# Kernel tuning notes

Hardware: AMD Instinct MI355X
Metric: run time of the kernel (lower is better)

The kernel has to match this reference:

```python
import jax, jax.numpy as jnp
import numpy as np

EMBED = 1024
HEAD = 128

def setup_inputs() -> dict:
    key = jax.random.key(0)
    k1, k2, k3, k4 = jax.random.split(key, 4)
    x = jax.random.normal(k1, (4, 4096, EMBED), dtype=jnp.float32)
    # nn.Linear default init ~ U(-1/sqrt(fan_in), 1/sqrt(fan_in)); weights stored as [in, out] for x @ W
    s = 1.0 / np.sqrt(EMBED)
    Wq = jax.random.uniform(k2, (EMBED, HEAD), dtype=jnp.float32, minval=-s, maxval=s)
    Wk = jax.random.uniform(k3, (EMBED, HEAD), dtype=jnp.float32, minval=-s, maxval=s)
    Wv = jax.random.uniform(k4, (EMBED, HEAD), dtype=jnp.float32, minval=-s, maxval=s)
    return {"x": x, "Wq": Wq, "Wk": Wk, "Wv": Wv}

def reference(x, Wq, Wk, Wv):
    # x: [B, S, E]
    B, S, E = x.shape
    q = x @ Wq  # [B, S, H]
    k = x @ Wk
    v = x @ Wv
    scale = jnp.asarray(k.shape[-1], x.dtype) ** -0.5
    scores = jnp.einsum('bqh,bkh->bqk', q, k) * scale  # [B, S, S]
    causal = jnp.tril(jnp.ones((S, S), dtype=bool))
    scores = jnp.where(causal, scores, jnp.asarray(-jnp.inf, x.dtype))
    attn = jax.nn.softmax(scores, axis=-1)
    return jnp.einsum('bqk,bkh->bqh', attn, v)  # [B, S, H]
```

## Files before the change

kernel.cpp:

```cpp
#include <hip/hip_runtime.h>
#include <math.h>

#define BATCH 4
#define SEQ   4096
#define EMB   1024
#define HD    128
#define MROWS (BATCH*SEQ)
#define SCALE 0.08838834764831844f
#define NJOBS 204
#define MAXC  6

typedef __attribute__((ext_vector_type(8))) short bf16x8;
typedef __attribute__((ext_vector_type(4))) short short4v;
typedef __attribute__((ext_vector_type(4))) float f32x4;
typedef __attribute__((ext_vector_type(4))) int   i32x4;

static __device__ __forceinline__ unsigned short f2bf(float f) {
    unsigned int u = __float_as_uint(f);
    u += 0x7fff + ((u >> 16) & 1);
    return (unsigned short)(u >> 16);
}
static __device__ __forceinline__ float bf2f(unsigned short s) {
    return __uint_as_float((unsigned int)s << 16);
}

__global__ __launch_bounds__(128) void wtrans_kernel(
    const float* __restrict__ Wq, const float* __restrict__ Wk,
    const float* __restrict__ Wv, unsigned short* __restrict__ Wt)
{
    const int w  = blockIdx.y;
    const float* W = (w == 0) ? Wq : (w == 1) ? Wk : Wv;
    const float sc = (w == 0) ? SCALE : 1.0f;
    unsigned short* dst = Wt + (size_t)w * 131072;
    const int n  = threadIdx.x;
    const int k0 = blockIdx.x * 64;
    for (int jc = 0; jc < 8; ++jc) {
        i32x4 p;
#pragma unroll
        for (int e = 0; e < 4; ++e) {
            float lo = W[(size_t)(k0 + jc * 8 + e * 2)     * HD + n] * sc;
            float hi = W[(size_t)(k0 + jc * 8 + e * 2 + 1) * HD + n] * sc;
            p[e] = (unsigned int)f2bf(lo) | ((unsigned int)f2bf(hi) << 16);
        }
        *(i32x4*)&dst[(size_t)n * 1024 + k0 + jc * 8] = p;
    }
}

__global__ __launch_bounds__(512, 4) void qkv_kernel(
    const float* __restrict__ x, const unsigned short* __restrict__ Wt,
    unsigned short* __restrict__ qb, unsigned short* __restrict__ kb,
    unsigned short* __restrict__ vtb)
{
    __shared__ __align__(16) unsigned short lds[32 * 72 + 384 * 72];
    unsigned short* xs = lds;
    unsigned short* Ws = lds + 32 * 72;

    const int t    = threadIdx.x;
    const int lane = t & 63, ng = t >> 6;
    const int quad = lane >> 4, l16 = lane & 15;
    const int m0   = blockIdx.x * 32;

    f32x4 acc[2][3];
#pragma unroll
    for (int i = 0; i < 2; ++i)
#pragma unroll
        for (int j = 0; j < 3; ++j) acc[i][j] = (f32x4){0.f, 0.f, 0.f, 0.f};

    const int xrow = t >> 4, xc4 = t & 15;
    const int wrow = t >> 3, wseg = t & 7;

    for (int kt = 0; kt < EMB; kt += 64) {
        __syncthreads();
        {
            float4 xa = *(const float4*)&x[(size_t)(m0 + xrow) * EMB + kt + xc4 * 4];
            short4v xcv;
            xcv[0] = (short)f2bf(xa.x); xcv[1] = (short)f2bf(xa.y);
            xcv[2] = (short)f2bf(xa.z); xcv[3] = (short)f2bf(xa.w);
            *(short4v*)&xs[xrow * 72 + xc4 * 4] = xcv;
        }
#pragma unroll
        for (int i = 0; i < 6; ++i) {
            int row = i * 64 + wrow;
            *(i32x4*)&Ws[row * 72 + wseg * 8] =
                *(const i32x4*)&Wt[(size_t)row * 1024 + kt + wseg * 8];
        }
        __syncthreads();
#pragma unroll
        for (int ks = 0; ks < 2; ++ks) {
            bf16x8 aA[2], aB[3];
#pragma unroll
            for (int mt = 0; mt < 2; ++mt)
                aA[mt] = *(const bf16x8*)&xs[(mt * 16 + l16) * 72 + ks * 32 + quad * 8];
#pragma unroll
            for (int jt = 0; jt < 3; ++jt)
                aB[jt] = *(const bf16x8*)&Ws[((ng * 3 + jt) * 16 + l16) * 72 + ks * 32 + quad * 8];
#pragma unroll
            for (int mt = 0; mt < 2; ++mt)
#pragma unroll
                for (int jt = 0; jt < 3; ++jt)
                    acc[mt][jt] = __builtin_amdgcn_mfma_f32_16x16x32_bf16(
                        aA[mt], aB[jt], acc[mt][jt], 0, 0, 0);
        }
    }

    __syncthreads();
    unsigned short* Cq = lds;
    unsigned short* Ck = lds + 32 * 136;
    unsigned short* Cv = lds + 2 * 32 * 136;
#pragma unroll
    for (int mt = 0; mt < 2; ++mt)
#pragma unroll
        for (int jt = 0; jt < 3; ++jt) {
            int nt = ng * 3 + jt;
            int wm = nt >> 3, nl = nt & 7;
            if (wm < 2) {
                unsigned short* C = (wm == 0) ? Cq : Ck;
#pragma unroll
                for (int rr = 0; rr < 4; ++rr)
                    C[(mt * 16 + quad * 4 + rr) * 136 + nl * 16 + l16] =
                        f2bf(acc[mt][jt][rr]);
            } else {
                short4v p;
                p[0] = (short)f2bf(acc[mt][jt][0]); p[1] = (short)f2bf(acc[mt][jt][1]);
                p[2] = (short)f2bf(acc[mt][jt][2]); p[3] = (short)f2bf(acc[mt][jt][3]);
                *(short4v*)&Cv[(nl * 16 + l16) * 40 + mt * 16 + quad * 4] = p;
            }
        }
    __syncthreads();
    {
        int row = t >> 4, seg = t & 15;
        *(i32x4*)&qb[((size_t)(m0 + row)) * HD + seg * 8] = *(const i32x4*)&Cq[row * 136 + seg * 8];
        *(i32x4*)&kb[((size_t)(m0 + row)) * HD + seg * 8] = *(const i32x4*)&Ck[row * 136 + seg * 8];
    }
    {
        const int b = m0 >> 12, s0 = m0 & 4095;
        int h = t >> 2, seg = t & 3;
        *(i32x4*)&vtb[(size_t)b * (HD * SEQ) + (size_t)h * SEQ + s0 + seg * 8] =
            *(const i32x4*)&Cv[h * 40 + seg * 8];
    }
}

#define PADK 136
#define PADV 72
#define PADP 72

__global__ __launch_bounds__(256, 3) void flash_kernel(
    const unsigned short* __restrict__ qb, const unsigned short* __restrict__ kb,
    const unsigned short* __restrict__ vtb, unsigned short* __restrict__ Opart,
    float* __restrict__ mbuf, float* __restrict__ lbuf)
{
    __shared__ __align__(16) unsigned short Ks[64 * PADK];
    __shared__ __align__(16) unsigned short Vt[128 * PADV];
    __shared__ __align__(16) unsigned short Pt[64 * PADP];

    const int t    = threadIdx.x;
    const int lane = t & 63, w = t >> 6;
    const int quad = lane >> 4, l16 = lane & 15;
    const int b    = blockIdx.y;

    const int j = blockIdx.x;
    int g = 0, s = 0;
#pragma unroll
    for (int gg = 0; gg < 5; ++gg)
        if (j >= s + 12 * (g + 1)) { s += 12 * (g + 1); ++g; }
    const int idx = j - s;
    const int qi  = 12 * g + idx / (g + 1);
    const int c   = idx % (g + 1);

    const int qrow = qi * 64 + w * 16 + l16;
    const int jbeg = c * 12;
    const int jend = min(jbeg + 12, qi + 1);

    bf16x8 qf[4];
    {
        const unsigned short* qp = qb + ((size_t)b * SEQ + qrow) * HD;
#pragma unroll
        for (int ks = 0; ks < 4; ++ks)
            qf[ks] = *(const bf16x8*)&qp[ks * 32 + quad * 8];
    }

    f32x4 O[8];
#pragma unroll
    for (int i = 0; i < 8; ++i) O[i] = (f32x4){0.f, 0.f, 0.f, 0.f};
    float m_run = -1e30f, l_run = 0.f;

    const unsigned short* kbb  = kb  + (size_t)b * SEQ * HD;
    const unsigned short* vtbb = vtb + (size_t)b * HD * SEQ;

    for (int j0 = jbeg; j0 < jend; ++j0) {
        __syncthreads();
#pragma unroll
        for (int i = 0; i < 4; ++i) {
            int gg = i * 256 + t;
            i32x4 kd = *(const i32x4*)&kbb[(size_t)j0 * 64 * HD + (size_t)gg * 8];
            *(i32x4*)&Ks[(gg >> 4) * PADK + (gg & 15) * 8] = kd;
        }
#pragma unroll
        for (int i = 0; i < 4; ++i) {
            int gg = i * 256 + t;
            i32x4 vd = *(const i32x4*)&vtbb[(size_t)(gg >> 3) * SEQ + j0 * 64 + (gg & 7) * 8];
            *(i32x4*)&Vt[(gg >> 3) * PADV + (gg & 7) * 8] = vd;
        }
        __syncthreads();

        f32x4 st[4];
#pragma unroll
        for (int mt = 0; mt < 4; ++mt) {
            f32x4 a = (f32x4){0.f, 0.f, 0.f, 0.f};
#pragma unroll
            for (int ks = 0; ks < 4; ++ks) {
                bf16x8 kf = *(const bf16x8*)&Ks[(mt * 16 + l16) * PADK + ks * 32 + quad * 8];
                a = __builtin_amdgcn_mfma_f32_16x16x32_bf16(kf, qf[ks], a, 0, 0, 0);
            }
            st[mt] = a;
        }

        if (j0 * 64 + 63 > qi * 64 + w * 16) {
#pragma unroll
            for (int mt = 0; mt < 4; ++mt)
#pragma unroll
                for (int rr = 0; rr < 4; ++rr) {
                    int kv = j0 * 64 + mt * 16 + quad * 4 + rr;
                    if (kv > qrow) st[mt][rr] = -1e30f;
                }
        }

        float mx = -1e30f;
#pragma unroll
        for (int mt = 0; mt < 4; ++mt)
#pragma unroll
            for (int rr = 0; rr < 4; ++rr) mx = fmaxf(mx, st[mt][rr]);
        mx = fmaxf(mx, __shfl_xor(mx, 16));
        mx = fmaxf(mx, __shfl_xor(mx, 32));
        const float m_new = fmaxf(m_run, mx);
        const float alpha = __expf(m_run - m_new);
        float psum = 0.f;
#pragma unroll
        for (int mt = 0; mt < 4; ++mt)
#pragma unroll
            for (int rr = 0; rr < 4; ++rr) {
                float p = __expf(st[mt][rr] - m_new);
                st[mt][rr] = p;
                psum += p;
            }
        psum += __shfl_xor(psum, 16);
        psum += __shfl_xor(psum, 32);
        m_run = m_new;
        l_run = l_run * alpha + psum;

#pragma unroll
        for (int mt = 0; mt < 4; ++mt) {
            short4v p;
            p[0] = (short)f2bf(st[mt][0]); p[1] = (short)f2bf(st[mt][1]);
            p[2] = (short)f2bf(st[mt][2]); p[3] = (short)f2bf(st[mt][3]);
            *(short4v*)&Pt[(w * 16 + l16) * PADP + mt * 16 + quad * 4] = p;
        }

#pragma unroll
        for (int i = 0; i < 8; ++i) {
            O[i][0] *= alpha; O[i][1] *= alpha; O[i][2] *= alpha; O[i][3] *= alpha;
        }

        bf16x8 pf0 = *(const bf16x8*)&Pt[(w * 16 + l16) * PADP + quad * 8];
        bf16x8 pf1 = *(const bf16x8*)&Pt[(w * 16 + l16) * PADP + 32 + quad * 8];
#pragma unroll
        for (int mt = 0; mt < 8; ++mt) {
            bf16x8 vf0 = *(const bf16x8*)&Vt[(mt * 16 + l16) * PADV + quad * 8];
            bf16x8 vf1 = *(const bf16x8*)&Vt[(mt * 16 + l16) * PADV + 32 + quad * 8];
            O[mt] = __builtin_amdgcn_mfma_f32_16x16x32_bf16(vf0, pf0, O[mt], 0, 0, 0);
            O[mt] = __builtin_amdgcn_mfma_f32_16x16x32_bf16(vf1, pf1, O[mt], 0, 0, 0);
        }
    }

    const int r = w * 16 + l16;
    const size_t jobbase = (size_t)b * NJOBS + j;
    unsigned short* po = Opart + jobbase * (64 * 128) + (size_t)r * 128;
#pragma unroll
    for (int mt = 0; mt < 8; ++mt) {
        short4v p;
        p[0] = (short)f2bf(O[mt][0]); p[1] = (short)f2bf(O[mt][1]);
        p[2] = (short)f2bf(O[mt][2]); p[3] = (short)f2bf(O[mt][3]);
        *(short4v*)&po[mt * 16 + quad * 4] = p;
    }
    if (quad == 0) {
        mbuf[jobbase * 64 + r] = m_run;
        lbuf[jobbase * 64 + r] = l_run;
    }
}

__global__ __launch_bounds__(256) void combine_kernel(
    const unsigned short* __restrict__ Opart, const float* __restrict__ mbuf,
    const float* __restrict__ lbuf, float* __restrict__ out)
{
    const int qi = blockIdx.x, b = blockIdx.y;
    const int g  = qi / 12;
    const int nc = g + 1;
    const int j0 = 6 * g * (g + 1) + (qi - 12 * g) * (g + 1);
    const int t = threadIdx.x;
    const int row = t >> 2, cg = (t & 3) * 32;

    float mv[MAXC], lv[MAXC];
    float M = -1e30f;
    for (int c2 = 0; c2 < nc; ++c2) {
        const size_t jb = (size_t)b * NJOBS + j0 + c2;
        mv[c2] = mbuf[jb * 64 + row];
        lv[c2] = lbuf[jb * 64 + row];
        M = fmaxf(M, mv[c2]);
    }
    float L = 0.f;
    for (int c2 = 0; c2 < nc; ++c2) L += __expf(mv[c2] - M) * lv[c2];
    const float Linv = 1.0f / L;

    float acc[32];
#pragma unroll
    for (int i = 0; i < 32; ++i) acc[i] = 0.f;
    for (int c2 = 0; c2 < nc; ++c2) {
        const float wgt = __expf(mv[c2] - M) * Linv;
        const unsigned short* po = Opart + ((size_t)b * NJOBS + j0 + c2) * (64 * 128) +
                                   (size_t)row * 128 + cg;
#pragma unroll
        for (int i = 0; i < 4; ++i) {
            i32x4 d = *(const i32x4*)&po[i * 8];
#pragma unroll
            for (int e = 0; e < 4; ++e) {
                unsigned int u = (unsigned int)d[e];
                acc[i * 8 + e * 2]     = fmaf(wgt, bf2f((unsigned short)(u & 0xffff)), acc[i * 8 + e * 2]);
                acc[i * 8 + e * 2 + 1] = fmaf(wgt, bf2f((unsigned short)(u >> 16)),   acc[i * 8 + e * 2 + 1]);
            }
        }
    }
    float* op = out + ((size_t)b * SEQ + qi * 64 + row) * HD + cg;
#pragma unroll
    for (int i = 0; i < 8; ++i) {
        float4 res;
        res.x = acc[i * 4]; res.y = acc[i * 4 + 1];
        res.z = acc[i * 4 + 2]; res.w = acc[i * 4 + 3];
        *(float4*)&op[i * 4] = res;
    }
}

extern "C" void kernel_launch(void* const* d_in, const int* in_sizes, int n_in,
                              void* d_out, int out_size, void* d_ws, size_t ws_size,
                              hipStream_t stream) {
    const float* x  = (const float*)d_in[0];
    const float* Wq = (const float*)d_in[1];
    const float* Wk = (const float*)d_in[2];
    const float* Wv = (const float*)d_in[3];

    unsigned short* qb    = (unsigned short*)d_ws;
    unsigned short* kb    = qb  + (size_t)MROWS * HD;
    unsigned short* vtb   = kb  + (size_t)MROWS * HD;
    unsigned short* Wt    = vtb + (size_t)MROWS * HD;
    unsigned short* Opart = Wt  + (size_t)3 * HD * EMB;
    float* mbuf = (float*)(Opart + (size_t)BATCH * NJOBS * 64 * 128);
    float* lbuf = mbuf + (size_t)BATCH * NJOBS * 64;
    float* out = (float*)d_out;

    wtrans_kernel <<<dim3(16, 3),    dim3(128), 0, stream>>>(Wq, Wk, Wv, Wt);
    qkv_kernel    <<<dim3(512),      dim3(512), 0, stream>>>(x, Wt, qb, kb, vtb);
    flash_kernel  <<<dim3(NJOBS, 4), dim3(256), 0, stream>>>(qb, kb, vtb, Opart, mbuf, lbuf);
    combine_kernel<<<dim3(64, 4),    dim3(256), 0, stream>>>(Opart, mbuf, lbuf, out);
}
```

Measured before the change: 186.7 us.

## Use 128-row query tiles, double-buffer x in QKV, coalesce weight transpose

The flash kernel now processes 128 query rows per 512-thread block, so each loaded K/V tile is shared by twice as many queries. Work is split into 10-tile chunks with a new job mapping interleaved across batches, and warps skip tiles that lie entirely above the causal diagonal. The QKV projection double-buffers the x tile, prefetching the next slice during MFMA compute, and drops one barrier per iteration. The weight transpose goes through LDS for coalesced reads, and the combine kernel is adjusted to the new partition layout. Larger blocks may lower occupancy and leave the work per block less even.

```diff
diff --git a/kernel.cpp b/kernel.cpp
--- a/kernel.cpp
+++ b/kernel.cpp
@@ -7,8 +7,9 @@
 #define HD    128
 #define MROWS (BATCH*SEQ)
 #define SCALE 0.08838834764831844f
-#define NJOBS 204
-#define MAXC  6
+#define CHUNK 10
+#define NJOBS 119
+#define MAXC  7
 
 typedef __attribute__((ext_vector_type(8))) short bf16x8;
 typedef __attribute__((ext_vector_type(4))) short short4v;
@@ -24,26 +25,38 @@
     return __uint_as_float((unsigned int)s << 16);
 }
 
-__global__ __launch_bounds__(128) void wtrans_kernel(
+__global__ __launch_bounds__(256) void wtrans_kernel(
     const float* __restrict__ Wq, const float* __restrict__ Wk,
     const float* __restrict__ Wv, unsigned short* __restrict__ Wt)
 {
+    __shared__ __align__(16) unsigned short Xs[16 * 132];
     const int w  = blockIdx.y;
     const float* W = (w == 0) ? Wq : (w == 1) ? Wk : Wv;
     const float sc = (w == 0) ? SCALE : 1.0f;
     unsigned short* dst = Wt + (size_t)w * 131072;
-    const int n  = threadIdx.x;
-    const int k0 = blockIdx.x * 64;
-    for (int jc = 0; jc < 8; ++jc) {
-        i32x4 p;
-#pragma unroll
-        for (int e = 0; e < 4; ++e) {
-            float lo = W[(size_t)(k0 + jc * 8 + e * 2)     * HD + n] * sc;
-            float hi = W[(size_t)(k0 + jc * 8 + e * 2 + 1) * HD + n] * sc;
-            p[e] = (unsigned int)f2bf(lo) | ((unsigned int)f2bf(hi) << 16);
-        }
-        *(i32x4*)&dst[(size_t)n * 1024 + k0 + jc * 8] = p;
-    }
+    const int k0 = blockIdx.x * 16;
+    const int t  = threadIdx.x;
+
+#pragma unroll
+    for (int i = 0; i < 2; ++i) {
+        int gg = i * 256 + t;
+        int row = gg >> 5, c4 = gg & 31;
+        float4 a = *(const float4*)&W[(size_t)(k0 + row) * HD + c4 * 4];
+        short4v p;
+        p[0] = (short)f2bf(a.x * sc); p[1] = (short)f2bf(a.y * sc);
+        p[2] = (short)f2bf(a.z * sc); p[3] = (short)f2bf(a.w * sc);
+        *(short4v*)&Xs[row * 132 + c4 * 4] = p;
+    }
+    __syncthreads();
+    const int n = t >> 1, half = t & 1;
+    i32x4 o;
+#pragma unroll
+    for (int e = 0; e < 4; ++e) {
+        unsigned int lo = Xs[(half * 8 + e * 2    ) * 132 + n];
+        unsigned int hi = Xs[(half * 8 + e * 2 + 1) * 132 + n];
+        o[e] = (int)(lo | (hi << 16));
+    }
+    *(i32x4*)&dst[(size_t)n * 1024 + k0 + half * 8] = o;
 }
 
 __global__ __launch_bounds__(512, 4) void qkv_kernel(
@@ -51,9 +64,10 @@
     unsigned short* __restrict__ qb, unsigned short* __restrict__ kb,
     unsigned short* __restrict__ vtb)
 {
-    __shared__ __align__(16) unsigned short lds[32 * 72 + 384 * 72];
-    unsigned short* xs = lds;
-    unsigned short* Ws = lds + 32 * 72;
+    __shared__ __align__(16) unsigned short lds[2 * 2304 + 384 * 72];
+    unsigned short* xs0 = lds;
+    unsigned short* xs1 = lds + 2304;
+    unsigned short* Ws  = lds + 4608;
 
     const int t    = threadIdx.x;
     const int lane = t & 63, ng = t >> 6;
@@ -66,31 +80,45 @@
 #pragma unroll
         for (int j = 0; j < 3; ++j) acc[i][j] = (f32x4){0.f, 0.f, 0.f, 0.f};
 
-    const int xrow = t >> 4, xc4 = t & 15;
-    const int wrow = t >> 3, wseg = t & 7;
+    const int xrow = t >> 3, xseg = t & 7;
+    if (t < 256) {
+        float4 a = *(const float4*)&x[(size_t)(m0 + xrow) * EMB + xseg * 8];
+        float4 b2 = *(const float4*)&x[(size_t)(m0 + xrow) * EMB + xseg * 8 + 4];
+        i32x4 p;
+        p[0] = (int)((unsigned)f2bf(a.x) | ((unsigned)f2bf(a.y) << 16));
+        p[1] = (int)((unsigned)f2bf(a.z) | ((unsigned)f2bf(a.w) << 16));
+        p[2] = (int)((unsigned)f2bf(b2.x) | ((unsigned)f2bf(b2.y) << 16));
+        p[3] = (int)((unsigned)f2bf(b2.z) | ((unsigned)f2bf(b2.w) << 16));
+        *(i32x4*)&xs0[xrow * 72 + xseg * 8] = p;
+    }
+    __syncthreads();
 
     for (int kt = 0; kt < EMB; kt += 64) {
-        __syncthreads();
-        {
-            float4 xa = *(const float4*)&x[(size_t)(m0 + xrow) * EMB + kt + xc4 * 4];
-            short4v xcv;
-            xcv[0] = (short)f2bf(xa.x); xcv[1] = (short)f2bf(xa.y);
-            xcv[2] = (short)f2bf(xa.z); xcv[3] = (short)f2bf(xa.w);
-            *(short4v*)&xs[xrow * 72 + xc4 * 4] = xcv;
-        }
+        unsigned short* xb = (kt & 64) ? xs1 : xs0;
+        unsigned short* xn = (kt & 64) ? xs0 : xs1;
 #pragma unroll
         for (int i = 0; i < 6; ++i) {
-            int row = i * 64 + wrow;
-            *(i32x4*)&Ws[row * 72 + wseg * 8] =
-                *(const i32x4*)&Wt[(size_t)row * 1024 + kt + wseg * 8];
-        }
-        __syncthreads();
+            int rowl = ng * 48 + i * 8 + (lane >> 3);
+            int seg  = lane & 7;
+            *(i32x4*)&Ws[rowl * 72 + seg * 8] =
+                *(const i32x4*)&Wt[(size_t)rowl * 1024 + kt + seg * 8];
+        }
+        if (t < 256 && kt + 64 < EMB) {
+            float4 a = *(const float4*)&x[(size_t)(m0 + xrow) * EMB + kt + 64 + xseg * 8];
+            float4 b2 = *(const float4*)&x[(size_t)(m0 + xrow) * EMB + kt + 64 + xseg * 8 + 4];
+            i32x4 p;
+            p[0] = (int)((unsigned)f2bf(a.x) | ((unsigned)f2bf(a.y) << 16));
+            p[1] = (int)((unsigned)f2bf(a.z) | ((unsigned)f2bf(a.w) << 16));
+            p[2] = (int)((unsigned)f2bf(b2.x) | ((unsigned)f2bf(b2.y) << 16));
+            p[3] = (int)((unsigned)f2bf(b2.z) | ((unsigned)f2bf(b2.w) << 16));
+            *(i32x4*)&xn[xrow * 72 + xseg * 8] = p;
+        }
 #pragma unroll
         for (int ks = 0; ks < 2; ++ks) {
             bf16x8 aA[2], aB[3];
 #pragma unroll
             for (int mt = 0; mt < 2; ++mt)
-                aA[mt] = *(const bf16x8*)&xs[(mt * 16 + l16) * 72 + ks * 32 + quad * 8];
+                aA[mt] = *(const bf16x8*)&xb[(mt * 16 + l16) * 72 + ks * 32 + quad * 8];
 #pragma unroll
             for (int jt = 0; jt < 3; ++jt)
                 aB[jt] = *(const bf16x8*)&Ws[((ng * 3 + jt) * 16 + l16) * 72 + ks * 32 + quad * 8];
@@ -101,9 +129,9 @@
                     acc[mt][jt] = __builtin_amdgcn_mfma_f32_16x16x32_bf16(
                         aA[mt], aB[jt], acc[mt][jt], 0, 0, 0);
         }
-    }
-
-    __syncthreads();
+        __syncthreads();
+    }
+
     unsigned short* Cq = lds;
     unsigned short* Ck = lds + 32 * 136;
     unsigned short* Cv = lds + 2 * 32 * 136;
@@ -144,32 +172,36 @@
 #define PADV 72
 #define PADP 72
 
-__global__ __launch_bounds__(256, 3) void flash_kernel(
+__global__ __launch_bounds__(512, 4) void flash_kernel(
     const unsigned short* __restrict__ qb, const unsigned short* __restrict__ kb,
     const unsigned short* __restrict__ vtb, unsigned short* __restrict__ Opart,
     float* __restrict__ mbuf, float* __restrict__ lbuf)
 {
     __shared__ __align__(16) unsigned short Ks[64 * PADK];
     __shared__ __align__(16) unsigned short Vt[128 * PADV];
-    __shared__ __align__(16) unsigned short Pt[64 * PADP];
+    __shared__ __align__(16) unsigned short Pt[128 * PADP];
+
+    const int bx   = blockIdx.x;
+    const int slot = bx & 7, pp = bx >> 3;
+    const int b    = slot >> 1;
+    const int jj   = pp * 2 + (slot & 1);
+    if (jj >= NJOBS) return;
 
     const int t    = threadIdx.x;
     const int lane = t & 63, w = t >> 6;
     const int quad = lane >> 4, l16 = lane & 15;
-    const int b    = blockIdx.y;
-
-    const int j = blockIdx.x;
-    int g = 0, s = 0;
-#pragma unroll
-    for (int gg = 0; gg < 5; ++gg)
-        if (j >= s + 12 * (g + 1)) { s += 12 * (g + 1); ++g; }
-    const int idx = j - s;
-    const int qi  = 12 * g + idx / (g + 1);
-    const int c   = idx % (g + 1);
-
-    const int qrow = qi * 64 + w * 16 + l16;
-    const int jbeg = c * 12;
-    const int jend = min(jbeg + 12, qi + 1);
+
+    int qi = 0, s = 0;
+    for (qi = 0; qi < 32; ++qi) {
+        int cnt = (qi + 5) / 5;
+        if (jj < s + cnt) break;
+        s += cnt;
+    }
+    const int c    = jj - s;
+    const int qrow = qi * 128 + w * 16 + l16;
+    const int jmax = 2 * qi + 2;
+    const int jbeg = c * CHUNK;
+    const int jend = min(jbeg + CHUNK, jmax);
 
     bf16x8 qf[4];
     {
@@ -190,18 +222,20 @@
     for (int j0 = jbeg; j0 < jend; ++j0) {
         __syncthreads();
 #pragma unroll
-        for (int i = 0; i < 4; ++i) {
-            int gg = i * 256 + t;
+        for (int i = 0; i < 2; ++i) {
+            int gg = i * 512 + t;
             i32x4 kd = *(const i32x4*)&kbb[(size_t)j0 * 64 * HD + (size_t)gg * 8];
             *(i32x4*)&Ks[(gg >> 4) * PADK + (gg & 15) * 8] = kd;
         }
 #pragma unroll
-        for (int i = 0; i < 4; ++i) {
-            int gg = i * 256 + t;
+        for (int i = 0; i < 2; ++i) {
+            int gg = i * 512 + t;
             i32x4 vd = *(const i32x4*)&vtbb[(size_t)(gg >> 3) * SEQ + j0 * 64 + (gg & 7) * 8];
             *(i32x4*)&Vt[(gg >> 3) * PADV + (gg & 7) * 8] = vd;
         }
         __syncthreads();
+
+        if (j0 * 64 > qi * 128 + w * 16 + 15) continue;
 
         f32x4 st[4];
 #pragma unroll
@@ -215,7 +249,7 @@
             st[mt] = a;
         }
 
-        if (j0 * 64 + 63 > qi * 64 + w * 16) {
+        if (j0 * 64 + 63 > qi * 128 + w * 16) {
 #pragma unroll
             for (int mt = 0; mt < 4; ++mt)
 #pragma unroll
@@ -273,8 +307,8 @@
     }
 
     const int r = w * 16 + l16;
-    const size_t jobbase = (size_t)b * NJOBS + j;
-    unsigned short* po = Opart + jobbase * (64 * 128) + (size_t)r * 128;
+    const size_t jobbase = (size_t)b * NJOBS + jj;
+    unsigned short* po = Opart + jobbase * (128 * 128) + (size_t)r * 128;
 #pragma unroll
     for (int mt = 0; mt < 8; ++mt) {
         short4v p;
@@ -283,53 +317,61 @@
         *(short4v*)&po[mt * 16 + quad * 4] = p;
     }
     if (quad == 0) {
-        mbuf[jobbase * 64 + r] = m_run;
-        lbuf[jobbase * 64 + r] = l_run;
-    }
-}
-
-__global__ __launch_bounds__(256) void combine_kernel(
+        mbuf[jobbase * 128 + r] = m_run;
+        lbuf[jobbase * 128 + r] = l_run;
+    }
+}
+
+__global__ __launch_bounds__(512) void combine_kernel(
     const unsigned short* __restrict__ Opart, const float* __restrict__ mbuf,
     const float* __restrict__ lbuf, float* __restrict__ out)
 {
     const int qi = blockIdx.x, b = blockIdx.y;
-    const int g  = qi / 12;
-    const int nc = g + 1;
-    const int j0 = 6 * g * (g + 1) + (qi - 12 * g) * (g + 1);
+    const int nc = (qi + 5) / 5;
+    int j0 = 0;
+    for (int q = 0; q < qi; ++q) j0 += (q + 5) / 5;
     const int t = threadIdx.x;
     const int row = t >> 2, cg = (t & 3) * 32;
 
     float mv[MAXC], lv[MAXC];
     float M = -1e30f;
-    for (int c2 = 0; c2 < nc; ++c2) {
-        const size_t jb = (size_t)b * NJOBS + j0 + c2;
-        mv[c2] = mbuf[jb * 64 + row];
-        lv[c2] = lbuf[jb * 64 + row];
-        M = fmaxf(M, mv[c2]);
+#pragma unroll
+    for (int c2 = 0; c2 < MAXC; ++c2) {
+        if (c2 < nc) {
+            const size_t jb = (size_t)b * NJOBS + j0 + c2;
+            mv[c2] = mbuf[jb * 128 + row];
+            lv[c2] = lbuf[jb * 128 + row];
+            M = fmaxf(M, mv[c2]);
+        } else { mv[c2] = -1e30f; lv[c2] = 0.f; }
     }
     float L = 0.f;
-    for (int c2 = 0; c2 < nc; ++c2) L += __expf(mv[c2] - M) * lv[c2];
+#pragma unroll
+    for (int c2 = 0; c2 < MAXC; ++c2)
+        if (c2 < nc) L += __expf(mv[c2] - M) * lv[c2];
     const float Linv = 1.0f / L;
 
     float acc[32];
 #pragma unroll
     for (int i = 0; i < 32; ++i) acc[i] = 0.f;
-    for (int c2 = 0; c2 < nc; ++c2) {
-        const float wgt = __expf(mv[c2] - M) * Linv;
-        const unsigned short* po = Opart + ((size_t)b * NJOBS + j0 + c2) * (64 * 128) +
-                                   (size_t)row * 128 + cg;
-#pragma unroll
-        for (int i = 0; i < 4; ++i) {
-            i32x4 d = *(const i32x4*)&po[i * 8];
-#pragma unroll
-            for (int e = 0; e < 4; ++e) {
-                unsigned int u = (unsigned int)d[e];
-                acc[i * 8 + e * 2]     = fmaf(wgt, bf2f((unsigned short)(u & 0xffff)), acc[i * 8 + e * 2]);
-                acc[i * 8 + e * 2 + 1] = fmaf(wgt, bf2f((unsigned short)(u >> 16)),   acc[i * 8 + e * 2 + 1]);
+#pragma unroll
+    for (int c2 = 0; c2 < MAXC; ++c2) {
+        if (c2 < nc) {
+            const float wgt = __expf(mv[c2] - M) * Linv;
+            const unsigned short* po = Opart + ((size_t)b * NJOBS + j0 + c2) * (128 * 128) +
+                                       (size_t)row * 128 + cg;
+#pragma unroll
+            for (int i = 0; i < 4; ++i) {
+                i32x4 d = *(const i32x4*)&po[i * 8];
+#pragma unroll
+                for (int e = 0; e < 4; ++e) {
+                    unsigned int u = (unsigned int)d[e];
+                    acc[i * 8 + e * 2]     = fmaf(wgt, bf2f((unsigned short)(u & 0xffff)), acc[i * 8 + e * 2]);
+                    acc[i * 8 + e * 2 + 1] = fmaf(wgt, bf2f((unsigned short)(u >> 16)),   acc[i * 8 + e * 2 + 1]);
+                }
             }
         }
     }
-    float* op = out + ((size_t)b * SEQ + qi * 64 + row) * HD + cg;
+    float* op = out + ((size_t)b * SEQ + qi * 128 + row) * HD + cg;
 #pragma unroll
     for (int i = 0; i < 8; ++i) {
         float4 res;
@@ -352,12 +394,12 @@
     unsigned short* vtb   = kb  + (size_t)MROWS * HD;
     unsigned short* Wt    = vtb + (size_t)MROWS * HD;
     unsigned short* Opart = Wt  + (size_t)3 * HD * EMB;
-    float* mbuf = (float*)(Opart + (size_t)BATCH * NJOBS * 64 * 128);
-    float* lbuf = mbuf + (size_t)BATCH * NJOBS * 64;
+    float* mbuf = (float*)(Opart + (size_t)BATCH * NJOBS * 128 * 128);
+    float* lbuf = mbuf + (size_t)BATCH * NJOBS * 128;
     float* out = (float*)d_out;
 
-    wtrans_kernel <<<dim3(16, 3),    dim3(128), 0, stream>>>(Wq, Wk, Wv, Wt);
-    qkv_kernel    <<<dim3(512),      dim3(512), 0, stream>>>(x, Wt, qb, kb, vtb);
-    flash_kernel  <<<dim3(NJOBS, 4), dim3(256), 0, stream>>>(qb, kb, vtb, Opart, mbuf, lbuf);
-    combine_kernel<<<dim3(64, 4),    dim3(256), 0, stream>>>(Opart, mbuf, lbuf, out);
-}
+    wtrans_kernel <<<dim3(64, 3),  dim3(256), 0, stream>>>(Wq, Wk, Wv, Wt);
+    qkv_kernel    <<<dim3(512),    dim3(512), 0, stream>>>(x, Wt, qb, kb, vtb);
+    flash_kernel  <<<dim3(480),    dim3(512), 0, stream>>>(qb, kb, vtb, Opart, mbuf, lbuf);
+    combine_kernel<<<dim3(32, 4),  dim3(512), 0, stream>>>(Opart, mbuf, lbuf, out);
+}
```

After: 167.8 us. 10.1% less time.
